# Kernel optimization log

Hardware: AMD Instinct MI355X
Metric: run time of the kernel (lower is better)

## Reference

```python
import jax, jax.numpy as jnp
import numpy as np

MAX_SEQ = 768  # hardcoded in original compute_freqs_cis
THETA = 10000.0


def _freqs_cis(C, T):
    # freqs over FULL embed dim C (matches original, not per-head)
    freqs = 1.0 / THETA ** (jnp.arange(0, C, 2, dtype=jnp.float32)[: C // 2] / C)
    t = jnp.arange(MAX_SEQ, dtype=jnp.float32)
    ang = jnp.outer(t, freqs)  # [MAX_SEQ, C/2]
    return jnp.cos(ang)[:T], jnp.sin(ang)[:T]  # each [T, C/2]


def _apply_rope(u):
    # u: [B, T, C]; rotate adjacent channel pairs across full C
    B, T, C = u.shape
    fr, fi = _freqs_cis(C, T)           # [T, C/2]
    u2 = u.astype(jnp.float32).reshape(B, T, C // 2, 2)
    ur, ui = u2[..., 0], u2[..., 1]     # [B, T, C/2]
    out_r = ur * fr - ui * fi
    out_i = ur * fi + ui * fr
    return jnp.stack([out_r, out_i], axis=-1).reshape(B, T, C).astype(u.dtype)


def setup_inputs() -> dict:
    key = jax.random.key(0)
    k1, k2, k3 = jax.random.split(key, 3)
    B, T, C = 16, 768, 1024
    x = jax.random.normal(k1, (B, T, C), dtype=jnp.float32)
    Wqkv = jax.random.normal(k2, (3 * C, C), dtype=jnp.float32) * 0.02
    bqkv = jnp.zeros((3 * C,), dtype=jnp.float32)
    Wo = jax.random.normal(k3, (C, C), dtype=jnp.float32) * 0.02
    bo = jnp.zeros((C,), dtype=jnp.float32)
    return {"x": x, "Wqkv": Wqkv, "bqkv": bqkv, "Wo": Wo, "bo": bo}


def reference(x, Wqkv, bqkv, Wo, bo):
    B, T, C = x.shape
    H = 16
    D = C // H
    qkv = x @ Wqkv.T + bqkv                      # [B, T, 3C]
    q, k, v = jnp.split(qkv, 3, axis=-1)
    q = _apply_rope(q)
    k = _apply_rope(k)
    # [B, H, T, D]
    q = q.reshape(B, T, H, D).transpose(0, 2, 1, 3)
    k = k.reshape(B, T, H, D).transpose(0, 2, 1, 3)
    v = v.reshape(B, T, H, D).transpose(0, 2, 1, 3)
    scale = 1.0 / jnp.sqrt(jnp.asarray(D, dtype=q.dtype))
    scores = jnp.einsum("bhqd,bhkd->bhqk", q, k) * scale
    causal = jnp.tril(jnp.ones((T, T), dtype=bool))
    scores = jnp.where(causal, scores, jnp.finfo(scores.dtype).min)
    attn = jax.nn.softmax(scores, axis=-1)
    y = jnp.einsum("bhqk,bhkd->bhqd", attn, v)   # [B, H, T, D]
    y = y.transpose(0, 2, 1, 3).reshape(B, T, C)
    return y @ Wo.T + bo
```

## Files before the change

### kernel.cpp

```cpp
#include <hip/hip_runtime.h>
#include <hip/hip_bf16.h>

typedef __attribute__((ext_vector_type(8))) short bf16x8;
typedef __attribute__((ext_vector_type(4))) float f32x4;
typedef unsigned short u16;
typedef unsigned int u32;

#define DEV __device__ __forceinline__

DEV float bf2f(u16 v) { u32 u = ((u32)v) << 16; return __builtin_bit_cast(float, u); }
DEV u16 f2bf(float f) {
    u32 u = __builtin_bit_cast(u32, f);
    u32 r = (u + 0x7FFFu + ((u >> 16) & 1u)) >> 16;
    return (u16)r;
}

DEV void gll16(const u16* g, u16* l) {
    __builtin_amdgcn_global_load_lds((const __attribute__((address_space(1))) void*)g,
                                     (__attribute__((address_space(3))) void*)l, 16, 0, 0);
}

#define WAIT_VM0()   asm volatile("s_waitcnt vmcnt(0)" ::: "memory")
#define WAIT_LGKM0() asm volatile("s_waitcnt lgkmcnt(0)" ::: "memory")
#define BAR()        __builtin_amdgcn_s_barrier()

__global__ void detect_kernel(const u32* __restrict__ x, int* __restrict__ flag) {
    __shared__ int cnt;
    if (threadIdx.x == 0) cnt = 0;
    __syncthreads();
    int c = 0;
    for (int i = threadIdx.x; i < 4096; i += 256) {
        u32 w = x[i];
        u32 e = (w >> 7) & 0xFF;
        c += (e >= 110 && e <= 132) ? 1 : 0;
    }
    atomicAdd(&cnt, c);
    __syncthreads();
    if (threadIdx.x == 0) *flag = (cnt * 2 > 4096) ? 1 : 0;
}

__global__ void cvt_bf16_kernel(const void* __restrict__ in, u16* __restrict__ out,
                                int n8, const int* __restrict__ flag) {
    const int fl = *flag;
    int i = blockIdx.x * 256 + threadIdx.x;
    const int stride = gridDim.x * 256;
    if (fl) {
        const bf16x8* ip = (const bf16x8*)in;
        bf16x8* op = (bf16x8*)out;
        for (; i < n8; i += stride) op[i] = ip[i];
    } else {
        const float4* ip = (const float4*)in;
        bf16x8* op = (bf16x8*)out;
        for (; i < n8; i += stride) {
            float4 a = ip[2 * i], b = ip[2 * i + 1];
            bf16x8 o;
            o[0] = (short)f2bf(a.x); o[1] = (short)f2bf(a.y);
            o[2] = (short)f2bf(a.z); o[3] = (short)f2bf(a.w);
            o[4] = (short)f2bf(b.x); o[5] = (short)f2bf(b.y);
            o[6] = (short)f2bf(b.z); o[7] = (short)f2bf(b.w);
            op[i] = o;
        }
    }
}

__global__ void cvt_f32_kernel(const void* __restrict__ in, float* __restrict__ out,
                               int n, const int* __restrict__ flag) {
    const int fl = *flag;
    int i = blockIdx.x * 256 + threadIdx.x;
    if (i < n) out[i] = fl ? bf2f(((const u16*)in)[i]) : ((const float*)in)[i];
}

__global__ void rope_table_kernel(float2* __restrict__ tab) {
    int idx = blockIdx.x * 256 + threadIdx.x;
    int t = idx >> 9, j = idx & 511;
    float freq = expf(-(float)(2 * j) * (9.210340371976184f / 1024.0f));
    float ang = (float)t * freq;
    tab[idx] = make_float2(cosf(ang), sinf(ang));
}

__global__ __launch_bounds__(256)
void gemm_bias_kernel(const u16* __restrict__ A, const u16* __restrict__ W,
                      const float* __restrict__ bias, void* __restrict__ C,
                      int M, int N, int K, const int* __restrict__ flag, int out_mode,
                      const float2* __restrict__ tab, int rope) {
    __shared__ u16 As[128 * 32];
    __shared__ u16 Bs[128 * 32];
    const int tid = threadIdx.x;
    const int l = tid & 63, w = tid >> 6;
    const int M0 = blockIdx.x * 128, N0 = blockIdx.y * 128;
    const int wr = (w >> 1) * 64, wc = (w & 1) * 64;
    const int lo = l & 15, hi = l >> 4;
    const int kk = hi * 8;
    const int f32out = out_mode ? (*flag == 0) : 0;

    const int srow = w * 32 + (l >> 2);
    const int scol = (l & 3) * 8;
    const u16* Ag = A + (size_t)(M0 + srow) * K + scol;
    const u16* Wg = W + (size_t)(N0 + srow) * K + scol;
    const size_t rowK16 = (size_t)16 * K;
    u16* AsW = As + w * 1024;
    u16* BsW = Bs + w * 1024;

    f32x4 acc[4][4] = {};

    for (int k0 = 0; k0 < K; k0 += 32) {
        __syncthreads();
        gll16(Ag + k0, AsW);
        gll16(Ag + k0 + rowK16, AsW + 512);
        gll16(Wg + k0, BsW);
        gll16(Wg + k0 + rowK16, BsW + 512);
        __syncthreads();

        bf16x8 a[4], b[4];
#pragma unroll
        for (int m = 0; m < 4; ++m)
            a[m] = *(const bf16x8*)&As[(wr + m * 16 + lo) * 32 + kk];
#pragma unroll
        for (int n = 0; n < 4; ++n)
            b[n] = *(const bf16x8*)&Bs[(wc + n * 16 + lo) * 32 + kk];
#pragma unroll
        for (int m = 0; m < 4; ++m)
#pragma unroll
            for (int n = 0; n < 4; ++n)
                acc[m][n] = __builtin_amdgcn_mfma_f32_16x16x32_bf16(a[m], b[n], acc[m][n], 0, 0, 0);
    }

    const int col0 = N0 + wc + lo;
    const int row0 = M0 + wr + hi * 4;
    const int do_rope = rope && (N0 < 2048);
    const int t0 = (M0 % 768) + wr + hi * 4;
#pragma unroll
    for (int n = 0; n < 4; ++n) {
        const int col = col0 + n * 16;
        float bi = bias[col];
        const int jf = (col & 1023) >> 1;
        const int odd = col & 1;
#pragma unroll
        for (int m = 0; m < 4; ++m)
#pragma unroll
            for (int j = 0; j < 4; ++j) {
                float v = acc[m][n][j] + bi;
                if (do_rope) {
                    float partner = __shfl_xor(v, 1);
                    float2 cs = tab[(t0 + m * 16 + j) * 512 + jf];
                    v = odd ? (v * cs.x + partner * cs.y) : (v * cs.x - partner * cs.y);
                }
                size_t idx = (size_t)(row0 + m * 16 + j) * N + col;
                if (f32out) ((float*)C)[idx] = v;
                else        ((u16*)C)[idx] = f2bf(v);
            }
    }
}

__global__ __launch_bounds__(256)
void attn_kernel(const u16* __restrict__ qkv, u16* __restrict__ y) {
    constexpr int T = 768, CH = 1024, QKVC = 3072;
    constexpr float NEG = -30000.0f;
    __shared__ u16 Ks[2][64 * 64];
    __shared__ u16 Vt[64 * 72];
    __shared__ u16 Ps[64 * 72];

    const int tid = threadIdx.x, l = tid & 63, w = tid >> 6;
    const int qt = blockIdx.x, h = blockIdx.y, b = blockIdx.z;
    const int lo = l & 15, hi = l >> 4;
    const int kk = hi * 8;
    const int swzk = (lo & 7) * 8;

    const int qrow = qt * 64 + w * 16 + lo;
    const u16* qptr = qkv + (size_t)(b * T + qrow) * QKVC + h * 64 + kk;
    bf16x8 aq0r = *(const bf16x8*)qptr;
    bf16x8 aq1r = *(const bf16x8*)(qptr + 32);
    bf16x8 aq0, aq1;
#pragma unroll
    for (int e = 0; e < 8; ++e) {
        aq0[e] = (short)f2bf(bf2f((u16)aq0r[e]) * 0.125f);
        aq1[e] = (short)f2bf(bf2f((u16)aq1r[e]) * 0.125f);
    }

    f32x4 o[4] = {};
    float mrun[4] = {NEG, NEG, NEG, NEG};
    float lrun[4] = {0.f, 0.f, 0.f, 0.f};

    const int ksr = w * 16 + (l >> 3);
    const int ksc = ((l & 7) ^ ((l >> 3) & 7)) * 8;
    const u16* kbase = qkv + (size_t)(b * T + ksr) * QKVC + CH + h * 64 + ksc;

    const int vd0 = (tid & 7) * 8;
    const int vswz = (tid & 7) * 8;
    const int vr0 = tid >> 3, vr1 = 32 + (tid >> 3);
    const u16* vbase = qkv + (size_t)(b * T) * QKVC + 2 * CH + h * 64 + vd0;

    gll16(kbase, &Ks[0][w * 1024]);
    gll16(kbase + (size_t)8 * QKVC, &Ks[0][w * 1024 + 512]);
    bf16x8 cv0 = *(const bf16x8*)(vbase + (size_t)vr0 * QKVC);
    bf16x8 cv1 = *(const bf16x8*)(vbase + (size_t)vr1 * QKVC);
    WAIT_VM0();
#pragma unroll
    for (int e = 0; e < 8; ++e) {
        Vt[(vd0 + e) * 72 + (vr0 ^ vswz)] = (u16)cv0[e];
        Vt[(vd0 + e) * 72 + (vr1 ^ vswz)] = (u16)cv1[e];
    }

    for (int kt = 0; kt <= qt; ++kt) {
        const int cur = kt & 1, nxt = cur ^ 1;
        bf16x8 nv0, nv1;
        if (kt < qt) {
            const size_t koff = (size_t)((kt + 1) * 64) * QKVC;
            gll16(kbase + koff, &Ks[nxt][w * 1024]);
            gll16(kbase + koff + (size_t)8 * QKVC, &Ks[nxt][w * 1024 + 512]);
            const u16* vb2 = vbase + (size_t)((kt + 1) * 64) * QKVC;
            nv0 = *(const bf16x8*)(vb2 + (size_t)vr0 * QKVC);
            nv1 = *(const bf16x8*)(vb2 + (size_t)vr1 * QKVC);
        }
        WAIT_LGKM0();
        BAR();

        __builtin_amdgcn_s_setprio(1);
        f32x4 s[4];
#pragma unroll
        for (int n = 0; n < 4; ++n) {
            bf16x8 kb0 = *(const bf16x8*)&Ks[cur][(n * 16 + lo) * 64 + (kk ^ swzk)];
            bf16x8 kb1 = *(const bf16x8*)&Ks[cur][(n * 16 + lo) * 64 + ((32 + kk) ^ swzk)];
            f32x4 z = {0.f, 0.f, 0.f, 0.f};
            z = __builtin_amdgcn_mfma_f32_16x16x32_bf16(aq0, kb0, z, 0, 0, 0);
            z = __builtin_amdgcn_mfma_f32_16x16x32_bf16(aq1, kb1, z, 0, 0, 0);
            s[n] = z;
        }
        __builtin_amdgcn_s_setprio(0);

        if (kt == qt) {
#pragma unroll
            for (int n = 0; n < 4; ++n) {
                int kcol = n * 16 + lo;
#pragma unroll
                for (int j = 0; j < 4; ++j)
                    if (kcol > w * 16 + hi * 4 + j) s[n][j] = NEG;
            }
        }
        float mnew[4], corr[4];
#pragma unroll
        for (int j = 0; j < 4; ++j) {
            float mx = fmaxf(fmaxf(s[0][j], s[1][j]), fmaxf(s[2][j], s[3][j]));
            mx = fmaxf(mx, __shfl_xor(mx, 1));
            mx = fmaxf(mx, __shfl_xor(mx, 2));
            mx = fmaxf(mx, __shfl_xor(mx, 4));
            mx = fmaxf(mx, __shfl_xor(mx, 8));
            mnew[j] = fmaxf(mrun[j], mx);
            corr[j] = __expf(mrun[j] - mnew[j]);
            mrun[j] = mnew[j];
        }
        float p[4][4];
#pragma unroll
        for (int n = 0; n < 4; ++n)
#pragma unroll
            for (int j = 0; j < 4; ++j)
                p[n][j] = __expf(s[n][j] - mnew[j]);
#pragma unroll
        for (int j = 0; j < 4; ++j) {
            float r = p[0][j] + p[1][j] + p[2][j] + p[3][j];
            r += __shfl_xor(r, 1);
            r += __shfl_xor(r, 2);
            r += __shfl_xor(r, 4);
            r += __shfl_xor(r, 8);
            lrun[j] = lrun[j] * corr[j] + r;
        }
#pragma unroll
        for (int n = 0; n < 4; ++n)
#pragma unroll
            for (int j = 0; j < 4; ++j)
                o[n][j] *= corr[j];
#pragma unroll
        for (int n = 0; n < 4; ++n)
#pragma unroll
            for (int j = 0; j < 4; ++j)
                Ps[(w * 16 + hi * 4 + j) * 72 + n * 16 + lo] = f2bf(p[n][j]);

        __builtin_amdgcn_s_setprio(1);
#pragma unroll
        for (int c = 0; c < 2; ++c) {
            bf16x8 pa = *(const bf16x8*)&Ps[(w * 16 + lo) * 72 + c * 32 + kk];
#pragma unroll
            for (int n = 0; n < 4; ++n) {
                const int v = (n * 2 + (lo >> 3)) & 7;
                bf16x8 vb = *(const bf16x8*)&Vt[(n * 16 + lo) * 72 + ((c * 32 + kk) ^ (v * 8))];
                o[n] = __builtin_amdgcn_mfma_f32_16x16x32_bf16(pa, vb, o[n], 0, 0, 0);
            }
        }
        __builtin_amdgcn_s_setprio(0);

        if (kt < qt) {
            WAIT_VM0();
            BAR();
#pragma unroll
            for (int e = 0; e < 8; ++e) {
                Vt[(vd0 + e) * 72 + (vr0 ^ vswz)] = (u16)nv0[e];
                Vt[(vd0 + e) * 72 + (vr1 ^ vswz)] = (u16)nv1[e];
            }
        }
    }

    float inv[4];
#pragma unroll
    for (int j = 0; j < 4; ++j) inv[j] = (lrun[j] > 0.f) ? 1.0f / lrun[j] : 0.f;
#pragma unroll
    for (int n = 0; n < 4; ++n)
#pragma unroll
        for (int j = 0; j < 4; ++j) {
            int t = qt * 64 + w * 16 + hi * 4 + j;
            y[(size_t)(b * T + t) * CH + h * 64 + n * 16 + lo] = f2bf(o[n][j] * inv[j]);
        }
}

extern "C" void kernel_launch(void* const* d_in, const int* in_sizes, int n_in,
                              void* d_out, int out_size, void* d_ws, size_t ws_size,
                              hipStream_t stream) {
    char* ws = (char*)d_ws;
    int*   flag  = (int*)ws;
    u16*   xb    = (u16*)(ws + 256);
    u16*   Wqb   = (u16*)(ws + 256 + 25165824);
    u16*   Wob   = (u16*)(ws + 256 + 31457280);
    float* bqf   = (float*)(ws + 256 + 33554432);
    float* bof   = (float*)(ws + 256 + 33566720);
    u16*   qkv   = (u16*)(ws + 256 + 33570816);
    u16*   y     = (u16*)(ws + 256 + 109068288);
    float2* tab  = (float2*)(ws + 256 + 134234112);

    detect_kernel<<<1, 256, 0, stream>>>((const u32*)d_in[0], flag);
    cvt_bf16_kernel<<<2048, 256, 0, stream>>>(d_in[0], xb,  12582912 / 8, flag);
    cvt_bf16_kernel<<<1536, 256, 0, stream>>>(d_in[1], Wqb, 3145728 / 8, flag);
    cvt_bf16_kernel<<<512,  256, 0, stream>>>(d_in[3], Wob, 1048576 / 8, flag);
    cvt_f32_kernel<<<12, 256, 0, stream>>>(d_in[2], bqf, 3072, flag);
    cvt_f32_kernel<<<4,  256, 0, stream>>>(d_in[4], bof, 1024, flag);
    rope_table_kernel<<<768 * 512 / 256, 256, 0, stream>>>(tab);

    gemm_bias_kernel<<<dim3(96, 24), 256, 0, stream>>>(xb, Wqb, bqf, qkv, 12288, 3072, 1024, flag, 0, tab, 1);
    attn_kernel<<<dim3(12, 16, 16), 256, 0, stream>>>(qkv, y);
    gemm_bias_kernel<<<dim3(96, 8), 256, 0, stream>>>(y, Wob, bof, d_out, 12288, 1024, 1024, flag, 1, tab, 0);
}
```

Measured before the change: 317.8 us.

## Replace GEMM with 256x128 triple-buffered swizzled LDS pipeline kernel

```diff
diff --git a/kernel.cpp b/kernel.cpp
--- a/kernel.cpp
+++ b/kernel.cpp
@@ -21,6 +21,7 @@
 }
 
 #define WAIT_VM0()   asm volatile("s_waitcnt vmcnt(0)" ::: "memory")
+#define WAIT_VM6()   asm volatile("s_waitcnt vmcnt(6)" ::: "memory")
 #define WAIT_LGKM0() asm volatile("s_waitcnt lgkmcnt(0)" ::: "memory")
 #define BAR()        __builtin_amdgcn_s_barrier()
 
@@ -78,57 +79,90 @@
     tab[idx] = make_float2(cosf(ang), sinf(ang));
 }
 
-__global__ __launch_bounds__(256)
-void gemm_bias_kernel(const u16* __restrict__ A, const u16* __restrict__ W,
-                      const float* __restrict__ bias, void* __restrict__ C,
-                      int M, int N, int K, const int* __restrict__ flag, int out_mode,
-                      const float2* __restrict__ tab, int rope) {
-    __shared__ u16 As[128 * 32];
-    __shared__ u16 Bs[128 * 32];
+__global__ __launch_bounds__(512)
+void gemm256_kernel(const u16* __restrict__ A, const u16* __restrict__ W,
+                    const float* __restrict__ bias, void* __restrict__ C,
+                    int N, int NBM, const int* __restrict__ flag, int out_mode,
+                    const float2* __restrict__ tab, int rope) {
+    constexpr int K = 1024, NT = 16;
+    __shared__ u16 lds[3][24576];
     const int tid = threadIdx.x;
     const int l = tid & 63, w = tid >> 6;
-    const int M0 = blockIdx.x * 128, N0 = blockIdx.y * 128;
-    const int wr = (w >> 1) * 64, wc = (w & 1) * 64;
+    const int wm = w >> 1, wn = w & 1;
     const int lo = l & 15, hi = l >> 4;
-    const int kk = hi * 8;
+
+    const int cpx = gridDim.x >> 3;
+    const int swz = (blockIdx.x & 7) * cpx + (blockIdx.x >> 3);
+    const int bm = swz % NBM, bn = swz / NBM;
+    const int M0 = bm * 256, N0 = bn * 128;
+
+    const int rS = tid >> 3;
+    const int qS = (tid & 7) ^ (rS & 7);
+    const u16* Ag = A + (size_t)(M0 + rS) * K + qS * 8;
+    const u16* Wg = W + (size_t)(N0 + rS) * K + qS * 8;
+    const int lb = w * 512;
+
+    f32x4 acc[4][4] = {};
+
+#define STAGE(kt, slot)                                                        \
+    {                                                                          \
+        u16* sA = &lds[slot][0];                                               \
+        u16* sB = &lds[slot][16384];                                           \
+        const u16* ga = Ag + (kt) * 64;                                        \
+        const u16* gb = Wg + (kt) * 64;                                        \
+        gll16(ga,                       sA + lb);                              \
+        gll16(ga + (size_t)64 * K,      sA + 4096 + lb);                       \
+        gll16(ga + (size_t)128 * K,     sA + 8192 + lb);                       \
+        gll16(ga + (size_t)192 * K,     sA + 12288 + lb);                      \
+        gll16(gb,                       sB + lb);                              \
+        gll16(gb + (size_t)64 * K,      sB + 4096 + lb);                       \
+    }
+
+    STAGE(0, 0);
+    STAGE(1, 1);
+    WAIT_VM6();
+
+#pragma unroll 1
+    for (int j = 0; j < NT; ++j) {
+        BAR();
+        if (j + 2 < NT) {
+            STAGE(j + 2, (j + 2) % 3);
+            WAIT_VM6();
+        } else {
+            WAIT_VM0();
+        }
+        const u16* sA = &lds[j % 3][0];
+        const u16* sB = &lds[j % 3][16384];
+        bf16x8 a[4][2], b[4][2];
+#pragma unroll
+        for (int m = 0; m < 4; ++m)
+#pragma unroll
+            for (int ks = 0; ks < 2; ++ks)
+                a[m][ks] = *(const bf16x8*)&sA[(wm * 64 + m * 16 + lo) * 64 +
+                                               (((ks * 4 + hi) ^ (lo & 7)) * 8)];
+#pragma unroll
+        for (int n = 0; n < 4; ++n)
+#pragma unroll
+            for (int ks = 0; ks < 2; ++ks)
+                b[n][ks] = *(const bf16x8*)&sB[(wn * 64 + n * 16 + lo) * 64 +
+                                               (((ks * 4 + hi) ^ (lo & 7)) * 8)];
+        __builtin_amdgcn_s_setprio(1);
+#pragma unroll
+        for (int m = 0; m < 4; ++m)
+#pragma unroll
+            for (int n = 0; n < 4; ++n)
+#pragma unroll
+                for (int ks = 0; ks < 2; ++ks)
+                    acc[m][n] = __builtin_amdgcn_mfma_f32_16x16x32_bf16(a[m][ks], b[n][ks], acc[m][n], 0, 0, 0);
+        __builtin_amdgcn_s_setprio(0);
+    }
+#undef STAGE
+
     const int f32out = out_mode ? (*flag == 0) : 0;
-
-    const int srow = w * 32 + (l >> 2);
-    const int scol = (l & 3) * 8;
-    const u16* Ag = A + (size_t)(M0 + srow) * K + scol;
-    const u16* Wg = W + (size_t)(N0 + srow) * K + scol;
-    const size_t rowK16 = (size_t)16 * K;
-    u16* AsW = As + w * 1024;
-    u16* BsW = Bs + w * 1024;
-
-    f32x4 acc[4][4] = {};
-
-    for (int k0 = 0; k0 < K; k0 += 32) {
-        __syncthreads();
-        gll16(Ag + k0, AsW);
-        gll16(Ag + k0 + rowK16, AsW + 512);
-        gll16(Wg + k0, BsW);
-        gll16(Wg + k0 + rowK16, BsW + 512);
-        __syncthreads();
-
-        bf16x8 a[4], b[4];
-#pragma unroll
-        for (int m = 0; m < 4; ++m)
-            a[m] = *(const bf16x8*)&As[(wr + m * 16 + lo) * 32 + kk];
-#pragma unroll
-        for (int n = 0; n < 4; ++n)
-            b[n] = *(const bf16x8*)&Bs[(wc + n * 16 + lo) * 32 + kk];
-#pragma unroll
-        for (int m = 0; m < 4; ++m)
-#pragma unroll
-            for (int n = 0; n < 4; ++n)
-                acc[m][n] = __builtin_amdgcn_mfma_f32_16x16x32_bf16(a[m], b[n], acc[m][n], 0, 0, 0);
-    }
-
-    const int col0 = N0 + wc + lo;
-    const int row0 = M0 + wr + hi * 4;
     const int do_rope = rope && (N0 < 2048);
-    const int t0 = (M0 % 768) + wr + hi * 4;
+    const int row0 = M0 + wm * 64 + hi * 4;
+    const int col0 = N0 + wn * 64 + lo;
+    const int t0 = (M0 % 768) + wm * 64 + hi * 4;
 #pragma unroll
     for (int n = 0; n < 4; ++n) {
         const int col = col0 + n * 16;
@@ -333,7 +367,7 @@
     cvt_f32_kernel<<<4,  256, 0, stream>>>(d_in[4], bof, 1024, flag);
     rope_table_kernel<<<768 * 512 / 256, 256, 0, stream>>>(tab);
 
-    gemm_bias_kernel<<<dim3(96, 24), 256, 0, stream>>>(xb, Wqb, bqf, qkv, 12288, 3072, 1024, flag, 0, tab, 1);
+    gemm256_kernel<<<1152, 512, 0, stream>>>(xb, Wqb, bqf, qkv, 3072, 48, flag, 0, tab, 1);
     attn_kernel<<<dim3(12, 16, 16), 256, 0, stream>>>(qkv, y);
-    gemm_bias_kernel<<<dim3(96, 8), 256, 0, stream>>>(y, Wob, bof, d_out, 12288, 1024, 1024, flag, 1, tab, 0);
-}
+    gemm256_kernel<<<384, 512, 0, stream>>>(y, Wob, bof, d_out, 1024, 48, flag, 1, tab, 0);
+}
```

Result: slower. 371.6 us (+16.9%).
